# Optimization experiments

Hardware: AMD Instinct MI355X
Metric: run time of the kernel (lower is better)

## Reference

```python
import jax, jax.numpy as jnp
import numpy as np

KERNEL = 11
BERT_DIM = 768
B, S, T = 2, 16, 64
EPS = 1e-6  # cosine-similarity eps (matches nn.CosineSimilarity(eps=1e-06))
CLAMP_MIN = 1e-6


def _kernel_mus(n):
    mus = [1.0]
    if n == 1:
        return mus
    b = 2.0 / (n - 1)
    mus.append(1.0 - b / 2.0)
    for i in range(1, n - 1):
        mus.append(mus[i] - b)
    return mus

MU = jnp.asarray(_kernel_mus(KERNEL), dtype=jnp.float32)      # (K,)
SIGMA = jnp.asarray([0.001] + [0.1] * (KERNEL - 1), dtype=jnp.float32)  # (K,)


def setup_inputs() -> dict:
    key = jax.random.key(0)
    ks = jax.random.split(key, 8)
    s = 0.02
    return {
        "claim_reps": jax.random.normal(ks[0], (B, T, BERT_DIM), jnp.float32),
        "sentence_token_reps": jax.random.normal(ks[1], (B, S, T, BERT_DIM), jnp.float32),
        "claim_token_mask": jnp.ones((B, T), dtype=bool),
        "token_mask": jnp.ones((B, S, T), dtype=bool),
        "w_sel": jax.random.normal(ks[2], (KERNEL, 1), jnp.float32) * s,
        "b_sel": jnp.zeros((1,), jnp.float32),
        "w_g1": jax.random.normal(ks[3], (2 * BERT_DIM, 128), jnp.float32) * s,
        "b_g1": jnp.zeros((128,), jnp.float32),
        "w_g2": jax.random.normal(ks[4], (128, 1), jnp.float32) * s,
        "b_g2": jnp.zeros((1,), jnp.float32),
        "w_rat": jax.random.normal(ks[5], (KERNEL, 1), jnp.float32) * s,
        "b_rat": jnp.zeros((1,), jnp.float32),
        "w_lab": jax.random.normal(ks[6], (2 * BERT_DIM, 3), jnp.float32) * s,
        "b_lab": jnp.zeros((3,), jnp.float32),
    }


def _forward(claim_reps, reps, token_mask,
             w_sel, b_sel, w_g1, b_g1, w_g2, b_g2, w_rat, b_rat, w_lab, b_lab):
    maskf = token_mask.astype(jnp.float32)           # (B,S,T)
    b_, s_, t_, d_ = reps.shape

    # ---------------- edge kernel ----------------
    # sim[b,i,j,p,q] = cos(reps[b,i,p], reps[b,j,q])
    norms = jnp.linalg.norm(reps, axis=-1)           # (B,S,T)
    dot = jnp.einsum('bipd,bjqd->bijpq', reps, reps)  # (B,S1,S2,T1,T2)
    sim = dot / jnp.maximum(norms[:, :, None, :, None] * norms[:, None, :, None, :], EPS)
    rbf = jnp.exp(-0.5 * ((sim[..., None] - MU) / SIGMA) ** 2)   # (B,S1,S2,T1,T2,K)
    # original mask broadcasts mask[b,s2,t1] over the summed T2 axis
    pool = rbf.sum(axis=4) * maskf[:, None, :, :, None]           # (B,S1,S2,T1,K)
    Ke = jnp.log(jnp.clip(pool, CLAMP_MIN, None))
    logits = Ke @ w_sel + b_sel                                   # (B,S1,S2,T1,1)
    m2 = jnp.broadcast_to(token_mask[:, None, :, :, None], logits.shape)
    attn = jax.nn.softmax(jnp.where(m2, logits, -10000.0), axis=3)  # softmax over T1
    # reps_exp[b,i,j,t,:] = reps[b,j,t,:]
    z_hat = jnp.einsum('bjtd,bijt->bijd', reps, attn[..., 0])     # (B,S1,S2,D)
    z = reps[:, :, 0, :]                                          # (B,S,D) CLS tokens
    z_exp = jnp.broadcast_to(z[:, None, :, :], z_hat.shape)       # z[b,s2]
    h = jax.nn.relu(jnp.concatenate([z_exp, z_hat], axis=-1) @ w_g1 + b_g1)
    beta = jax.nn.softmax(h @ w_g2 + b_g2, axis=1)                # softmax over S1
    v = jnp.concatenate([jnp.sum(beta * z_hat, axis=1), z], axis=-1)  # (B,S,2D)
    sentence_label_pred = jax.nn.softmax(v @ w_lab + b_lab, axis=-1)  # (B,S,3)

    # ---------------- node kernel ----------------
    # NOTE: the original broadcasts BOTH operands over t2, so sim depends only on
    # (b,s,t1): cos(claim[b,t1], reps[b,s,t1]); the T2 sum multiplies by n_token.
    nc = jnp.linalg.norm(claim_reps, axis=-1)                     # (B,T)
    dotn = jnp.einsum('btd,bstd->bst', claim_reps, reps)          # (B,S,T)
    simn = dotn / jnp.maximum(nc[:, None, :] * norms, EPS)
    rbfn = jnp.exp(-0.5 * ((simn[..., None] - MU) / SIGMA) ** 2)  # (B,S,T,K)
    pooln = rbfn * maskf[..., None] * jnp.float32(t_)
    phi = jnp.mean(jnp.log(jnp.clip(pooln, CLAMP_MIN, None)), axis=-2)  # (B,S,K)
    rationale = jax.nn.softmax(phi @ w_rat + b_rat, axis=1)       # (B,S,1)

    return jnp.sum(sentence_label_pred * rationale, axis=1)       # (B,3)


def reference(claim_reps, sentence_token_reps, claim_token_mask, token_mask,
              w_sel, b_sel, w_g1, b_g1, w_g2, b_g2, w_rat, b_rat, w_lab, b_lab):
    # claim_token_mask is accepted by the original forward but never used
    return _forward(claim_reps, sentence_token_reps, token_mask,
                    w_sel, b_sel, w_g1, b_g1, w_g2, b_g2,
                    w_rat, b_rat, w_lab, b_lab)
```

## Files before the change

kernel.cpp:

```cpp
#include <hip/hip_runtime.h>
#include <hip/hip_bf16.h>

#define NK 11

typedef __bf16 bf16_t;
typedef __bf16 bf16x4 __attribute__((ext_vector_type(4)));
typedef __bf16 bf16x8 __attribute__((ext_vector_type(8)));
typedef float f32x4 __attribute__((ext_vector_type(4)));

__device__ __constant__ float MU_C[NK]   = {1.0f,0.9f,0.7f,0.5f,0.3f,0.1f,-0.1f,-0.3f,-0.5f,-0.7f,-0.9f};
__device__ __constant__ float ISIG_C[NK] = {1000.0f,10.0f,10.0f,10.0f,10.0f,10.0f,10.0f,10.0f,10.0f,10.0f,10.0f};

__global__ __launch_bounds__(256) void kp_prep(
    const float* __restrict__ reps, const float* __restrict__ b_rat,
    bf16_t* __restrict__ repsb, float* __restrict__ norms,
    float* __restrict__ phir, float* __restrict__ out)
{
    const int tid = threadIdx.x;
    const int tok = blockIdx.x * 8 + (tid >> 5);
    const int ln  = tid & 31;
    const float* src = reps + (size_t)tok * 768 + ln * 24;
    bf16_t*      dst = repsb + (size_t)tok * 768 + ln * 24;
    float s = 0.f;
    #pragma unroll
    for (int x = 0; x < 24; x += 4) {
        f32x4 f = *(const f32x4*)(src + x);
        bf16x4 h = {(bf16_t)f[0], (bf16_t)f[1], (bf16_t)f[2], (bf16_t)f[3]};
        *(bf16x4*)(dst + x) = h;
        s += f[0]*f[0] + f[1]*f[1] + f[2]*f[2] + f[3]*f[3];
    }
    #pragma unroll
    for (int off = 16; off; off >>= 1) s += __shfl_xor(s, off, 32);
    if (ln == 0) norms[tok] = sqrtf(s);
    if (blockIdx.x == 0) {
        if (tid < 6) out[tid] = 0.f;
        if (tid >= 32 && tid < 64) phir[tid - 32] = b_rat[0];
    }
}

__global__ __launch_bounds__(256) void ka_simpool(
    const bf16_t* __restrict__ repsb, const float* __restrict__ norms,
    const float* __restrict__ w_sel, const float* __restrict__ b_sel,
    float* __restrict__ zhat)
{
    __shared__ __align__(16) bf16_t As[64*136];
    __shared__ __align__(16) bf16_t Bs[64*136];
    __shared__ float normI[64], normJ[64], logitsS[64], attnS[64];

    const int tid = threadIdx.x;
    const int bid = blockIdx.x;
    const int b = bid >> 8, rem = bid & 255, i = rem >> 4, j = rem & 15;
    const bf16_t* Rib = repsb + (size_t)((b*16 + i)*64) * 768;
    const bf16_t* Rjb = repsb + (size_t)((b*16 + j)*64) * 768;

    if (tid < 64)       normI[tid]    = norms[(b*16 + i)*64 + tid];
    else if (tid < 128) normJ[tid-64] = norms[(b*16 + j)*64 + (tid-64)];

    const int wave = tid >> 6, lane = tid & 63;
    const int wr = wave & 1, wc = wave >> 1;
    const int m16 = lane & 15, q4 = lane >> 4;

    f32x4 acc00 = {0.f,0.f,0.f,0.f}, acc01 = {0.f,0.f,0.f,0.f};
    f32x4 acc10 = {0.f,0.f,0.f,0.f}, acc11 = {0.f,0.f,0.f,0.f};

    const int c8 = (tid & 15) * 8;
    const int r0 = tid >> 4;

    for (int ko = 0; ko < 6; ++ko) {
        __syncthreads();
        #pragma unroll
        for (int p = 0; p < 4; ++p) {
            int row = r0 + 16*p;
            bf16x8 wa = *(const bf16x8*)(Rib + (size_t)row*768 + ko*128 + c8);
            bf16x8 wb = *(const bf16x8*)(Rjb + (size_t)row*768 + ko*128 + c8);
            *(bf16x8*)&As[row*136 + c8] = wa;
            *(bf16x8*)&Bs[row*136 + c8] = wb;
        }
        __syncthreads();
        #pragma unroll
        for (int ks = 0; ks < 4; ++ks) {
            int kb = ks*32 + q4*8;
            bf16x8 a0 = *(const bf16x8*)&As[(32*wr      + m16)*136 + kb];
            bf16x8 a1 = *(const bf16x8*)&As[(32*wr + 16 + m16)*136 + kb];
            bf16x8 b0 = *(const bf16x8*)&Bs[(32*wc      + m16)*136 + kb];
            bf16x8 b1 = *(const bf16x8*)&Bs[(32*wc + 16 + m16)*136 + kb];
            acc00 = __builtin_amdgcn_mfma_f32_16x16x32_bf16(a0, b0, acc00, 0, 0, 0);
            acc01 = __builtin_amdgcn_mfma_f32_16x16x32_bf16(a0, b1, acc01, 0, 0, 0);
            acc10 = __builtin_amdgcn_mfma_f32_16x16x32_bf16(a1, b0, acc10, 0, 0, 0);
            acc11 = __builtin_amdgcn_mfma_f32_16x16x32_bf16(a1, b1, acc11, 0, 0, 0);
        }
    }
    __syncthreads();

    float* simb = (float*)As;
    #pragma unroll
    for (int tr = 0; tr < 2; ++tr) {
        #pragma unroll
        for (int tc = 0; tc < 2; ++tc) {
            f32x4 a = (tr==0) ? ((tc==0)?acc00:acc01) : ((tc==0)?acc10:acc11);
            int q = 32*wc + 16*tc + m16;
            #pragma unroll
            for (int e = 0; e < 4; ++e) {
                int p = 32*wr + 16*tr + q4*4 + e;
                float v = a[e] / fmaxf(normI[p]*normJ[q], 1e-6f);
                if (i == j && p == q) v = 1.0f;
                simb[p*65 + q] = v;
            }
        }
    }
    __syncthreads();

    float* poolp = (float*)Bs;
    {
        int p = tid & 63, qg = tid >> 6;
        float sv[16];
        #pragma unroll
        for (int qi = 0; qi < 16; ++qi) sv[qi] = simb[p*65 + qg*16 + qi];
        #pragma unroll
        for (int k = 0; k < NK; ++k) {
            float mu = MU_C[k], is = ISIG_C[k], s = 0.f;
            #pragma unroll
            for (int qi = 0; qi < 16; ++qi) {
                float d = (sv[qi] - mu) * is;
                s += __expf(-0.5f*d*d);
            }
            poolp[(qg*64 + p)*NK + k] = s;
        }
    }
    __syncthreads();

    if (tid < 64) {
        int p = tid;
        float lg = b_sel[0];
        #pragma unroll
        for (int k = 0; k < NK; ++k) {
            float pool = poolp[p*NK+k] + poolp[(64+p)*NK+k]
                       + poolp[(128+p)*NK+k] + poolp[(192+p)*NK+k];
            lg += __logf(fmaxf(pool, 1e-6f)) * w_sel[k];
        }
        logitsS[p] = lg;
    }
    __syncthreads();
    if (tid < 64) {
        float x = logitsS[tid], m = x;
        #pragma unroll
        for (int off = 32; off; off >>= 1) m = fmaxf(m, __shfl_xor(m, off));
        float e = __expf(x - m), ssum = e;
        #pragma unroll
        for (int off = 32; off; off >>= 1) ssum += __shfl_xor(ssum, off);
        attnS[tid] = e / ssum;
    }
    __syncthreads();

    {
        float* zo = zhat + (size_t)bid * 768;
        #pragma unroll
        for (int rr = 0; rr < 3; ++rr) {
            int d = tid + 256*rr;
            float a = 0.f;
            #pragma unroll 8
            for (int t = 0; t < 64; ++t) a += attnS[t] * (float)Rjb[(size_t)t*768 + d];
            zo[d] = a;
        }
    }
}

__global__ __launch_bounds__(256) void kb_mid(
    const float* __restrict__ reps, const float* __restrict__ claim,
    const bf16_t* __restrict__ repsb, const float* __restrict__ norms,
    const float* __restrict__ zhat,
    const float* __restrict__ w_g1, const float* __restrict__ b_g1,
    const float* __restrict__ w_g2, const float* __restrict__ b_g2,
    const float* __restrict__ w_rat,
    float* __restrict__ g, float* __restrict__ phir)
{
    __shared__ float zl[768];
    __shared__ float zh[4][768];
    __shared__ float hz[2][128];
    __shared__ float hj[2][4][128];
    __shared__ float phiLoc;

    const int tid = threadIdx.x;
    const int bid = blockIdx.x;

    if (bid < 128) {
        const int b = bid >> 6, rem = bid & 63, i = rem >> 2, jg = rem & 3;
        const float* zsrc = reps + (size_t)((b*16 + i)*64) * 768;
        for (int d = tid; d < 768; d += 256) zl[d] = zsrc[d];
        #pragma unroll
        for (int jj = 0; jj < 4; ++jj)
            for (int d = tid; d < 768; d += 256)
                zh[jj][d] = zhat[(size_t)((b*16 + i)*16 + jg*4 + jj)*768 + d];
        __syncthreads();

        const int c = tid & 127, rh = tid >> 7;
        float accz = 0.f, a0 = 0.f, a1 = 0.f, a2 = 0.f, a3 = 0.f;
        const float* wz = w_g1 + (size_t)(rh*384)*128 + c;
        const float* wh = w_g1 + (size_t)(768 + rh*384)*128 + c;
        #pragma unroll 4
        for (int r = 0; r < 384; ++r) {
            float w0 = wz[(size_t)r*128];
            float w1 = wh[(size_t)r*128];
            int rr = rh*384 + r;
            accz += zl[rr]*w0;
            a0 += zh[0][rr]*w1; a1 += zh[1][rr]*w1;
            a2 += zh[2][rr]*w1; a3 += zh[3][rr]*w1;
        }
        hz[rh][c] = accz;
        hj[rh][0][c] = a0; hj[rh][1][c] = a1; hj[rh][2][c] = a2; hj[rh][3][c] = a3;
        __syncthreads();

        const int jj = tid >> 6, ln = tid & 63;
        float s = 0.f;
        #pragma unroll
        for (int cc = ln; cc < 128; cc += 64) {
            float h = hz[0][cc] + hz[1][cc] + hj[0][jj][cc] + hj[1][jj][cc] + b_g1[cc];
            s += fmaxf(h, 0.f) * w_g2[cc];
        }
        #pragma unroll
        for (int off = 32; off; off >>= 1) s += __shfl_xor(s, off);
        if (ln == 0) g[(b*16 + i)*16 + jg*4 + jj] = s + b_g2[0];
    } else {
        const int pid = bid - 128;
        const int b = pid >> 6, rem = pid & 63, s_ = rem >> 2, tg = rem & 3;
        if (tid == 0) phiLoc = 0.f;
        __syncthreads();
        const int tok = tg*16 + (tid >> 4), part = tid & 15;
        const float*  cp = claim + (size_t)(b*64 + tok)*768 + part*48;
        const bf16_t* rp = repsb + (size_t)((b*16 + s_)*64 + tok)*768 + part*48;
        float sd = 0.f, sc = 0.f;
        #pragma unroll
        for (int x = 0; x < 48; x += 8) {
            f32x4 c0 = *(const f32x4*)(cp + x);
            f32x4 c1 = *(const f32x4*)(cp + x + 4);
            bf16x8 r8 = *(const bf16x8*)(rp + x);
            sd += c0[0]*(float)r8[0] + c0[1]*(float)r8[1] + c0[2]*(float)r8[2] + c0[3]*(float)r8[3]
                + c1[0]*(float)r8[4] + c1[1]*(float)r8[5] + c1[2]*(float)r8[6] + c1[3]*(float)r8[7];
            sc += c0[0]*c0[0]+c0[1]*c0[1]+c0[2]*c0[2]+c0[3]*c0[3]
                + c1[0]*c1[0]+c1[1]*c1[1]+c1[2]*c1[2]+c1[3]*c1[3];
        }
        #pragma unroll
        for (int off = 8; off; off >>= 1) {
            sd += __shfl_xor(sd, off, 16);
            sc += __shfl_xor(sc, off, 16);
        }
        if (part == 0) {
            float nr = norms[(b*16 + s_)*64 + tok];
            float simn = sd / fmaxf(sqrtf(sc)*nr, 1e-6f);
            float contrib = 0.f;
            #pragma unroll
            for (int k = 0; k < NK; ++k) {
                float dd = (simn - MU_C[k]) * ISIG_C[k];
                float pool = __expf(-0.5f*dd*dd) * 64.0f;
                contrib += w_rat[k] * __logf(fmaxf(pool, 1e-6f));
            }
            atomicAdd(&phiLoc, contrib * (1.0f/64.0f));
        }
        __syncthreads();
        if (tid == 0) atomicAdd(&phir[b*16 + s_], phiLoc);
    }
}

__global__ __launch_bounds__(256) void kc_final(
    const float* __restrict__ reps, const float* __restrict__ zhat,
    const float* __restrict__ g, const float* __restrict__ phir,
    const float* __restrict__ w_lab, const float* __restrict__ b_lab,
    float* __restrict__ out)
{
    __shared__ float betaS[16], vs[768], zl[768], Lm[3];
    __shared__ float ratS;

    const int tid = threadIdx.x;
    const int b = blockIdx.x >> 4, j = blockIdx.x & 15;

    if (tid < 16) {
        float x = g[(b*16 + tid)*16 + j], m = x;
        #pragma unroll
        for (int off = 8; off; off >>= 1) m = fmaxf(m, __shfl_xor(m, off, 16));
        float e = __expf(x - m), ss = e;
        #pragma unroll
        for (int off = 8; off; off >>= 1) ss += __shfl_xor(ss, off, 16);
        betaS[tid] = e / ss;
    }
    for (int d = tid; d < 768; d += 256) zl[d] = reps[(size_t)((b*16 + j)*64)*768 + d];
    __syncthreads();

    for (int d = tid; d < 768; d += 256) {
        float s = 0.f;
        #pragma unroll
        for (int ii = 0; ii < 16; ++ii) s += betaS[ii] * zhat[(size_t)((b*16 + ii)*16 + j)*768 + d];
        vs[d] = s;
    }
    __syncthreads();

    if (tid < 192) {
        int m = tid >> 6, ln = tid & 63;
        float s = 0.f;
        #pragma unroll 4
        for (int d = ln; d < 768; d += 64)
            s += vs[d]*w_lab[(size_t)d*3 + m] + zl[d]*w_lab[(size_t)(768 + d)*3 + m];
        #pragma unroll
        for (int off = 32; off; off >>= 1) s += __shfl_xor(s, off);
        if (ln == 0) Lm[m] = s + b_lab[m];
    }
    if (tid >= 192 && tid < 208) {
        int s_ = tid - 192;
        float x = phir[b*16 + s_], m = x;
        #pragma unroll
        for (int off = 8; off; off >>= 1) m = fmaxf(m, __shfl_xor(m, off, 16));
        float e = __expf(x - m), ss = e;
        #pragma unroll
        for (int off = 8; off; off >>= 1) ss += __shfl_xor(ss, off, 16);
        if (s_ == j) ratS = e / ss;
    }
    __syncthreads();

    if (tid == 0) {
        float m = fmaxf(Lm[0], fmaxf(Lm[1], Lm[2]));
        float e0 = __expf(Lm[0]-m), e1 = __expf(Lm[1]-m), e2 = __expf(Lm[2]-m);
        float inv = 1.f / (e0+e1+e2);
        float r = ratS;
        atomicAdd(&out[b*3+0], r*e0*inv);
        atomicAdd(&out[b*3+1], r*e1*inv);
        atomicAdd(&out[b*3+2], r*e2*inv);
    }
}

extern "C" void kernel_launch(void* const* d_in, const int* in_sizes, int n_in,
                              void* d_out, int out_size, void* d_ws, size_t ws_size,
                              hipStream_t stream) {
    const float* claim = (const float*)d_in[0];
    const float* reps  = (const float*)d_in[1];
    const float* w_sel = (const float*)d_in[4];
    const float* b_sel = (const float*)d_in[5];
    const float* w_g1  = (const float*)d_in[6];
    const float* b_g1  = (const float*)d_in[7];
    const float* w_g2  = (const float*)d_in[8];
    const float* b_g2  = (const float*)d_in[9];
    const float* w_rat = (const float*)d_in[10];
    const float* b_rat = (const float*)d_in[11];
    const float* w_lab = (const float*)d_in[12];
    const float* b_lab = (const float*)d_in[13];

    float*  ws    = (float*)d_ws;
    bf16_t* repsb = (bf16_t*)d_ws;
    float*  norms = ws + 786432;
    float*  zhat  = ws + 786432 + 2048;
    float*  g     = ws + 786432 + 2048 + 393216;
    float*  phir  = ws + 786432 + 2048 + 393216 + 512;
    float*  out   = (float*)d_out;

    hipLaunchKernelGGL(kp_prep,    dim3(256), dim3(256), 0, stream,
                       reps, b_rat, repsb, norms, phir, out);
    hipLaunchKernelGGL(ka_simpool, dim3(512), dim3(256), 0, stream,
                       repsb, norms, w_sel, b_sel, zhat);
    hipLaunchKernelGGL(kb_mid,     dim3(256), dim3(256), 0, stream,
                       reps, claim, repsb, norms, zhat,
                       w_g1, b_g1, w_g2, b_g2, w_rat, g, phir);
    hipLaunchKernelGGL(kc_final,   dim3(32),  dim3(256), 0, stream,
                       reps, zhat, g, phir, w_lab, b_lab, out);
}
```

Before: 149.6 us.

## Fold gating MLP into final kernel with MFMA, store zhat in bf16

Removes the kb_mid kernel. The claim/rationale phi computation moves into extra blocks of ka_simpool, and the gating MLP (w_g1 projection) moves into kc_final as a bf16 MFMA GEMM over a pre-transposed bf16 copy of w_g1 built in kp_prep. zhat is now written in bf16 with vectorized 8-wide loads and a two-half reduction. This cuts one launch and halves zhat traffic, but gives kc_final only 32 blocks, each doing a serial 12-chunk GEMM, and adds bf16 rounding in the MLP.

```diff
diff --git a/kernel.cpp b/kernel.cpp
--- a/kernel.cpp
+++ b/kernel.cpp
@@ -12,43 +12,116 @@
 __device__ __constant__ float ISIG_C[NK] = {1000.0f,10.0f,10.0f,10.0f,10.0f,10.0f,10.0f,10.0f,10.0f,10.0f,10.0f};
 
 __global__ __launch_bounds__(256) void kp_prep(
-    const float* __restrict__ reps, const float* __restrict__ b_rat,
+    const float* __restrict__ reps, const float* __restrict__ w_g1,
+    const float* __restrict__ b_rat,
     bf16_t* __restrict__ repsb, float* __restrict__ norms,
-    float* __restrict__ phir, float* __restrict__ out)
+    bf16_t* __restrict__ w1t, float* __restrict__ phir, float* __restrict__ out)
 {
+    __shared__ bf16_t wt[128*137];
     const int tid = threadIdx.x;
-    const int tok = blockIdx.x * 8 + (tid >> 5);
-    const int ln  = tid & 31;
-    const float* src = reps + (size_t)tok * 768 + ln * 24;
-    bf16_t*      dst = repsb + (size_t)tok * 768 + ln * 24;
-    float s = 0.f;
-    #pragma unroll
-    for (int x = 0; x < 24; x += 4) {
-        f32x4 f = *(const f32x4*)(src + x);
-        bf16x4 h = {(bf16_t)f[0], (bf16_t)f[1], (bf16_t)f[2], (bf16_t)f[3]};
-        *(bf16x4*)(dst + x) = h;
-        s += f[0]*f[0] + f[1]*f[1] + f[2]*f[2] + f[3]*f[3];
-    }
-    #pragma unroll
-    for (int off = 16; off; off >>= 1) s += __shfl_xor(s, off, 32);
-    if (ln == 0) norms[tok] = sqrtf(s);
-    if (blockIdx.x == 0) {
-        if (tid < 6) out[tid] = 0.f;
-        if (tid >= 32 && tid < 64) phir[tid - 32] = b_rat[0];
+    const int bid = blockIdx.x;
+    if (bid < 256) {
+        const int tok = bid * 8 + (tid >> 5);
+        const int ln  = tid & 31;
+        const float* src = reps + (size_t)tok * 768 + ln * 24;
+        bf16_t*      dst = repsb + (size_t)tok * 768 + ln * 24;
+        float s = 0.f;
+        #pragma unroll
+        for (int x = 0; x < 24; x += 4) {
+            f32x4 f = *(const f32x4*)(src + x);
+            bf16x4 h = {(bf16_t)f[0], (bf16_t)f[1], (bf16_t)f[2], (bf16_t)f[3]};
+            *(bf16x4*)(dst + x) = h;
+            s += f[0]*f[0] + f[1]*f[1] + f[2]*f[2] + f[3]*f[3];
+        }
+        #pragma unroll
+        for (int off = 16; off; off >>= 1) s += __shfl_xor(s, off, 32);
+        if (ln == 0) norms[tok] = sqrtf(s);
+        if (bid == 0) {
+            if (tid < 6) out[tid] = 0.f;
+            if (tid >= 32 && tid < 64) phir[tid - 32] = b_rat[0];
+        }
+    } else {
+        const int td = bid - 256;
+        const float* wsrc = w_g1 + (size_t)td * 128 * 128;
+        #pragma unroll
+        for (int rep = 0; rep < 16; ++rep) {
+            int linear = rep*256 + tid;
+            int row = linear >> 5, c4 = (linear & 31) * 4;
+            f32x4 v = *(const f32x4*)(wsrc + (size_t)row*128 + c4);
+            wt[(c4+0)*137 + row] = (bf16_t)v[0];
+            wt[(c4+1)*137 + row] = (bf16_t)v[1];
+            wt[(c4+2)*137 + row] = (bf16_t)v[2];
+            wt[(c4+3)*137 + row] = (bf16_t)v[3];
+        }
+        __syncthreads();
+        #pragma unroll
+        for (int rep = 0; rep < 8; ++rep) {
+            int linear = rep*256 + tid;
+            int c = linear >> 4, d8 = (linear & 15) * 8;
+            bf16x8 h8;
+            #pragma unroll
+            for (int e = 0; e < 8; ++e) h8[e] = wt[c*137 + d8 + e];
+            *(bf16x8*)&w1t[(size_t)c*1536 + td*128 + d8] = h8;
+        }
     }
 }
 
 __global__ __launch_bounds__(256) void ka_simpool(
+    const float* __restrict__ claim,
     const bf16_t* __restrict__ repsb, const float* __restrict__ norms,
     const float* __restrict__ w_sel, const float* __restrict__ b_sel,
-    float* __restrict__ zhat)
+    const float* __restrict__ w_rat,
+    bf16_t* __restrict__ zhatb, float* __restrict__ phir)
 {
     __shared__ __align__(16) bf16_t As[64*136];
     __shared__ __align__(16) bf16_t Bs[64*136];
     __shared__ float normI[64], normJ[64], logitsS[64], attnS[64];
+    __shared__ float phiLoc;
 
     const int tid = threadIdx.x;
     const int bid = blockIdx.x;
+
+    if (bid >= 512) {
+        const int pid = bid - 512;
+        const int b = pid >> 6, rem = pid & 63, s_ = rem >> 2, tg = rem & 3;
+        if (tid == 0) phiLoc = 0.f;
+        __syncthreads();
+        const int tok = tg*16 + (tid >> 4), part = tid & 15;
+        const float*  cp = claim + (size_t)(b*64 + tok)*768 + part*48;
+        const bf16_t* rp = repsb + (size_t)((b*16 + s_)*64 + tok)*768 + part*48;
+        float sd = 0.f, sc = 0.f;
+        #pragma unroll
+        for (int x = 0; x < 48; x += 8) {
+            f32x4 c0 = *(const f32x4*)(cp + x);
+            f32x4 c1 = *(const f32x4*)(cp + x + 4);
+            bf16x8 r8 = *(const bf16x8*)(rp + x);
+            sd += c0[0]*(float)r8[0] + c0[1]*(float)r8[1] + c0[2]*(float)r8[2] + c0[3]*(float)r8[3]
+                + c1[0]*(float)r8[4] + c1[1]*(float)r8[5] + c1[2]*(float)r8[6] + c1[3]*(float)r8[7];
+            sc += c0[0]*c0[0]+c0[1]*c0[1]+c0[2]*c0[2]+c0[3]*c0[3]
+                + c1[0]*c1[0]+c1[1]*c1[1]+c1[2]*c1[2]+c1[3]*c1[3];
+        }
+        #pragma unroll
+        for (int off = 8; off; off >>= 1) {
+            sd += __shfl_xor(sd, off, 16);
+            sc += __shfl_xor(sc, off, 16);
+        }
+        if (part == 0) {
+            float nr = norms[(b*16 + s_)*64 + tok];
+            float simn = sd / fmaxf(sqrtf(sc)*nr, 1e-6f);
+            float contrib = 0.f;
+            #pragma unroll
+            for (int k = 0; k < NK; ++k) {
+                float dd = (simn - MU_C[k]) * ISIG_C[k];
+                float pool = __expf(-0.5f*dd*dd) * 64.0f;
+                contrib += w_rat[k] * __logf(fmaxf(pool, 1e-6f));
+            }
+            atomicAdd(&phiLoc, contrib * (1.0f/64.0f));
+        }
+        __syncthreads();
+        if (tid == 0) atomicAdd(&phir[b*16 + s_], phiLoc);
+        return;
+    }
+
     const int b = bid >> 8, rem = bid & 255, i = rem >> 4, j = rem & 15;
     const bf16_t* Rib = repsb + (size_t)((b*16 + i)*64) * 768;
     const bf16_t* Rjb = repsb + (size_t)((b*16 + j)*64) * 768;
@@ -153,128 +226,111 @@
     __syncthreads();
 
     {
-        float* zo = zhat + (size_t)bid * 768;
-        #pragma unroll
-        for (int rr = 0; rr < 3; ++rr) {
-            int d = tid + 256*rr;
-            float a = 0.f;
+        float a8[8] = {0.f,0.f,0.f,0.f,0.f,0.f,0.f,0.f};
+        const int th = (tid >= 96 && tid < 192) ? 1 : 0;
+        const int dg = tid - th*96;
+        if (tid < 192) {
+            const bf16_t* src = Rjb + dg*8 + (size_t)th*32*768;
             #pragma unroll 8
-            for (int t = 0; t < 64; ++t) a += attnS[t] * (float)Rjb[(size_t)t*768 + d];
-            zo[d] = a;
+            for (int t = 0; t < 32; ++t) {
+                bf16x8 r = *(const bf16x8*)(src + (size_t)t*768);
+                float at = attnS[th*32 + t];
+                #pragma unroll
+                for (int e = 0; e < 8; ++e) a8[e] += at * (float)r[e];
+            }
+        }
+        __syncthreads();
+        float* zp = (float*)As;
+        if (th == 1) {
+            #pragma unroll
+            for (int e = 0; e < 8; ++e) zp[dg*8 + e] = a8[e];
+        }
+        __syncthreads();
+        if (tid < 96) {
+            bf16x8 o;
+            #pragma unroll
+            for (int e = 0; e < 8; ++e) o[e] = (bf16_t)(a8[e] + zp[tid*8 + e]);
+            *(bf16x8*)&zhatb[(size_t)bid*768 + tid*8] = o;
         }
     }
 }
 
-__global__ __launch_bounds__(256) void kb_mid(
-    const float* __restrict__ reps, const float* __restrict__ claim,
-    const bf16_t* __restrict__ repsb, const float* __restrict__ norms,
-    const float* __restrict__ zhat,
-    const float* __restrict__ w_g1, const float* __restrict__ b_g1,
-    const float* __restrict__ w_g2, const float* __restrict__ b_g2,
-    const float* __restrict__ w_rat,
-    float* __restrict__ g, float* __restrict__ phir)
-{
-    __shared__ float zl[768];
-    __shared__ float zh[4][768];
-    __shared__ float hz[2][128];
-    __shared__ float hj[2][4][128];
-    __shared__ float phiLoc;
-
-    const int tid = threadIdx.x;
-    const int bid = blockIdx.x;
-
-    if (bid < 128) {
-        const int b = bid >> 6, rem = bid & 63, i = rem >> 2, jg = rem & 3;
-        const float* zsrc = reps + (size_t)((b*16 + i)*64) * 768;
-        for (int d = tid; d < 768; d += 256) zl[d] = zsrc[d];
-        #pragma unroll
-        for (int jj = 0; jj < 4; ++jj)
-            for (int d = tid; d < 768; d += 256)
-                zh[jj][d] = zhat[(size_t)((b*16 + i)*16 + jg*4 + jj)*768 + d];
-        __syncthreads();
-
-        const int c = tid & 127, rh = tid >> 7;
-        float accz = 0.f, a0 = 0.f, a1 = 0.f, a2 = 0.f, a3 = 0.f;
-        const float* wz = w_g1 + (size_t)(rh*384)*128 + c;
-        const float* wh = w_g1 + (size_t)(768 + rh*384)*128 + c;
-        #pragma unroll 4
-        for (int r = 0; r < 384; ++r) {
-            float w0 = wz[(size_t)r*128];
-            float w1 = wh[(size_t)r*128];
-            int rr = rh*384 + r;
-            accz += zl[rr]*w0;
-            a0 += zh[0][rr]*w1; a1 += zh[1][rr]*w1;
-            a2 += zh[2][rr]*w1; a3 += zh[3][rr]*w1;
-        }
-        hz[rh][c] = accz;
-        hj[rh][0][c] = a0; hj[rh][1][c] = a1; hj[rh][2][c] = a2; hj[rh][3][c] = a3;
-        __syncthreads();
-
-        const int jj = tid >> 6, ln = tid & 63;
-        float s = 0.f;
-        #pragma unroll
-        for (int cc = ln; cc < 128; cc += 64) {
-            float h = hz[0][cc] + hz[1][cc] + hj[0][jj][cc] + hj[1][jj][cc] + b_g1[cc];
-            s += fmaxf(h, 0.f) * w_g2[cc];
-        }
-        #pragma unroll
-        for (int off = 32; off; off >>= 1) s += __shfl_xor(s, off);
-        if (ln == 0) g[(b*16 + i)*16 + jg*4 + jj] = s + b_g2[0];
-    } else {
-        const int pid = bid - 128;
-        const int b = pid >> 6, rem = pid & 63, s_ = rem >> 2, tg = rem & 3;
-        if (tid == 0) phiLoc = 0.f;
-        __syncthreads();
-        const int tok = tg*16 + (tid >> 4), part = tid & 15;
-        const float*  cp = claim + (size_t)(b*64 + tok)*768 + part*48;
-        const bf16_t* rp = repsb + (size_t)((b*16 + s_)*64 + tok)*768 + part*48;
-        float sd = 0.f, sc = 0.f;
-        #pragma unroll
-        for (int x = 0; x < 48; x += 8) {
-            f32x4 c0 = *(const f32x4*)(cp + x);
-            f32x4 c1 = *(const f32x4*)(cp + x + 4);
-            bf16x8 r8 = *(const bf16x8*)(rp + x);
-            sd += c0[0]*(float)r8[0] + c0[1]*(float)r8[1] + c0[2]*(float)r8[2] + c0[3]*(float)r8[3]
-                + c1[0]*(float)r8[4] + c1[1]*(float)r8[5] + c1[2]*(float)r8[6] + c1[3]*(float)r8[7];
-            sc += c0[0]*c0[0]+c0[1]*c0[1]+c0[2]*c0[2]+c0[3]*c0[3]
-                + c1[0]*c1[0]+c1[1]*c1[1]+c1[2]*c1[2]+c1[3]*c1[3];
-        }
-        #pragma unroll
-        for (int off = 8; off; off >>= 1) {
-            sd += __shfl_xor(sd, off, 16);
-            sc += __shfl_xor(sc, off, 16);
-        }
-        if (part == 0) {
-            float nr = norms[(b*16 + s_)*64 + tok];
-            float simn = sd / fmaxf(sqrtf(sc)*nr, 1e-6f);
-            float contrib = 0.f;
-            #pragma unroll
-            for (int k = 0; k < NK; ++k) {
-                float dd = (simn - MU_C[k]) * ISIG_C[k];
-                float pool = __expf(-0.5f*dd*dd) * 64.0f;
-                contrib += w_rat[k] * __logf(fmaxf(pool, 1e-6f));
-            }
-            atomicAdd(&phiLoc, contrib * (1.0f/64.0f));
-        }
-        __syncthreads();
-        if (tid == 0) atomicAdd(&phir[b*16 + s_], phiLoc);
-    }
-}
-
 __global__ __launch_bounds__(256) void kc_final(
-    const float* __restrict__ reps, const float* __restrict__ zhat,
-    const float* __restrict__ g, const float* __restrict__ phir,
+    const float* __restrict__ reps, const bf16_t* __restrict__ zhatb,
+    const bf16_t* __restrict__ w1t,
+    const float* __restrict__ b_g1, const float* __restrict__ w_g2,
+    const float* __restrict__ b_g2, const float* __restrict__ phir,
     const float* __restrict__ w_lab, const float* __restrict__ b_lab,
     float* __restrict__ out)
 {
-    __shared__ float betaS[16], vs[768], zl[768], Lm[3];
+    __shared__ __align__(16) bf16_t Ws[128*136];
+    __shared__ __align__(16) bf16_t As[16*136];
+    __shared__ float gpart[4][16];
+    __shared__ float betaS[16], zl[768], vs[768], Lm[3];
     __shared__ float ratS;
 
     const int tid = threadIdx.x;
     const int b = blockIdx.x >> 4, j = blockIdx.x & 15;
-
+    const int wave = tid >> 6, lane = tid & 63;
+    const int m16 = lane & 15, q4 = lane >> 4;
+
+    for (int d = tid; d < 768; d += 256) zl[d] = reps[(size_t)((b*16 + j)*64)*768 + d];
+
+    f32x4 acc0 = {0.f,0.f,0.f,0.f}, acc1 = {0.f,0.f,0.f,0.f};
+    for (int ck = 0; ck < 12; ++ck) {
+        __syncthreads();
+        #pragma unroll
+        for (int rep = 0; rep < 8; ++rep) {
+            int linear = rep*256 + tid;
+            int c = linear >> 4, k8 = (linear & 15)*8;
+            *(bf16x8*)&Ws[c*136 + k8] = *(const bf16x8*)&w1t[(size_t)c*1536 + ck*128 + k8];
+        }
+        if (ck < 6) {
+            #pragma unroll
+            for (int rep = 0; rep < 2; ++rep) {
+                int linear = rep*256 + tid;
+                int ii = linear >> 5, c4 = (linear & 31)*4;
+                f32x4 v = *(const f32x4*)(reps + (size_t)((b*16 + ii)*64)*768 + ck*128 + c4);
+                bf16x4 h = {(bf16_t)v[0],(bf16_t)v[1],(bf16_t)v[2],(bf16_t)v[3]};
+                *(bf16x4*)&As[ii*136 + c4] = h;
+            }
+        } else {
+            int ii = tid >> 4, k8 = (tid & 15)*8;
+            *(bf16x8*)&As[ii*136 + k8] =
+                *(const bf16x8*)&zhatb[(size_t)((b*16 + ii)*16 + j)*768 + (ck-6)*128 + k8];
+        }
+        __syncthreads();
+        #pragma unroll
+        for (int ks = 0; ks < 4; ++ks) {
+            bf16x8 a  = *(const bf16x8*)&As[m16*136 + ks*32 + q4*8];
+            bf16x8 b0 = *(const bf16x8*)&Ws[(wave*32 + m16)*136 + ks*32 + q4*8];
+            bf16x8 b1 = *(const bf16x8*)&Ws[(wave*32 + 16 + m16)*136 + ks*32 + q4*8];
+            acc0 = __builtin_amdgcn_mfma_f32_16x16x32_bf16(a, b0, acc0, 0, 0, 0);
+            acc1 = __builtin_amdgcn_mfma_f32_16x16x32_bf16(a, b1, acc1, 0, 0, 0);
+        }
+    }
+    {
+        int c0 = wave*32 + m16, c1 = wave*32 + 16 + m16;
+        float bg0 = b_g1[c0], bg1 = b_g1[c1];
+        float wg0 = w_g2[c0], wg1 = w_g2[c1];
+        float ge[4];
+        #pragma unroll
+        for (int e = 0; e < 4; ++e)
+            ge[e] = fmaxf(acc0[e] + bg0, 0.f)*wg0 + fmaxf(acc1[e] + bg1, 0.f)*wg1;
+        #pragma unroll
+        for (int off = 1; off < 16; off <<= 1) {
+            #pragma unroll
+            for (int e = 0; e < 4; ++e) ge[e] += __shfl_xor(ge[e], off);
+        }
+        if (m16 == 0) {
+            #pragma unroll
+            for (int e = 0; e < 4; ++e) gpart[wave][q4*4 + e] = ge[e];
+        }
+    }
+    __syncthreads();
     if (tid < 16) {
-        float x = g[(b*16 + tid)*16 + j], m = x;
+        float x = gpart[0][tid] + gpart[1][tid] + gpart[2][tid] + gpart[3][tid] + b_g2[0];
+        float m = x;
         #pragma unroll
         for (int off = 8; off; off >>= 1) m = fmaxf(m, __shfl_xor(m, off, 16));
         float e = __expf(x - m), ss = e;
@@ -282,17 +338,34 @@
         for (int off = 8; off; off >>= 1) ss += __shfl_xor(ss, off, 16);
         betaS[tid] = e / ss;
     }
-    for (int d = tid; d < 768; d += 256) zl[d] = reps[(size_t)((b*16 + j)*64)*768 + d];
-    __syncthreads();
-
-    for (int d = tid; d < 768; d += 256) {
-        float s = 0.f;
-        #pragma unroll
-        for (int ii = 0; ii < 16; ++ii) s += betaS[ii] * zhat[(size_t)((b*16 + ii)*16 + j)*768 + d];
-        vs[d] = s;
-    }
-    __syncthreads();
-
+    __syncthreads();
+    {
+        float va[8] = {0.f,0.f,0.f,0.f,0.f,0.f,0.f,0.f};
+        const int ih = (tid >= 96 && tid < 192) ? 1 : 0;
+        const int dg = tid - ih*96;
+        if (tid < 192) {
+            const bf16_t* src = zhatb + (size_t)((b*16 + ih*8)*16 + j)*768 + dg*8;
+            #pragma unroll
+            for (int ii = 0; ii < 8; ++ii) {
+                bf16x8 r = *(const bf16x8*)(src + (size_t)ii*16*768);
+                float bt = betaS[ih*8 + ii];
+                #pragma unroll
+                for (int e = 0; e < 8; ++e) va[e] += bt * (float)r[e];
+            }
+        }
+        __syncthreads();
+        float* vsp = (float*)Ws;
+        if (ih == 1) {
+            #pragma unroll
+            for (int e = 0; e < 8; ++e) vsp[dg*8 + e] = va[e];
+        }
+        __syncthreads();
+        if (tid < 96) {
+            #pragma unroll
+            for (int e = 0; e < 8; ++e) vs[tid*8 + e] = va[e] + vsp[tid*8 + e];
+        }
+    }
+    __syncthreads();
     if (tid < 192) {
         int m = tid >> 6, ln = tid & 63;
         float s = 0.f;
@@ -314,7 +387,6 @@
         if (s_ == j) ratS = e / ss;
     }
     __syncthreads();
-
     if (tid == 0) {
         float m = fmaxf(Lm[0], fmaxf(Lm[1], Lm[2]));
         float e0 = __expf(Lm[0]-m), e1 = __expf(Lm[1]-m), e2 = __expf(Lm[2]-m);
@@ -343,20 +415,17 @@
     const float* b_lab = (const float*)d_in[13];
 
     float*  ws    = (float*)d_ws;
-    bf16_t* repsb = (bf16_t*)d_ws;
+    bf16_t* repsb = (bf16_t*)ws;
     float*  norms = ws + 786432;
-    float*  zhat  = ws + 786432 + 2048;
-    float*  g     = ws + 786432 + 2048 + 393216;
-    float*  phir  = ws + 786432 + 2048 + 393216 + 512;
+    bf16_t* zhatb = (bf16_t*)(ws + 786432 + 2048);
+    bf16_t* w1t   = (bf16_t*)(ws + 786432 + 2048 + 196608);
+    float*  phir  = ws + 786432 + 2048 + 196608 + 98304;
     float*  out   = (float*)d_out;
 
-    hipLaunchKernelGGL(kp_prep,    dim3(256), dim3(256), 0, stream,
-                       reps, b_rat, repsb, norms, phir, out);
-    hipLaunchKernelGGL(ka_simpool, dim3(512), dim3(256), 0, stream,
-                       repsb, norms, w_sel, b_sel, zhat);
-    hipLaunchKernelGGL(kb_mid,     dim3(256), dim3(256), 0, stream,
-                       reps, claim, repsb, norms, zhat,
-                       w_g1, b_g1, w_g2, b_g2, w_rat, g, phir);
+    hipLaunchKernelGGL(kp_prep,    dim3(268), dim3(256), 0, stream,
+                       reps, w_g1, b_rat, repsb, norms, w1t, phir, out);
+    hipLaunchKernelGGL(ka_simpool, dim3(640), dim3(256), 0, stream,
+                       claim, repsb, norms, w_sel, b_sel, w_rat, zhatb, phir);
     hipLaunchKernelGGL(kc_final,   dim3(32),  dim3(256), 0, stream,
-                       reps, zhat, g, phir, w_lab, b_lab, out);
+                       reps, zhatb, w1t, b_g1, w_g2, b_g2, phir, w_lab, b_lab, out);
 }
```

Measured after the change: 125.0 us. 1.2x faster.
